# Optimization experiments

Hardware: AMD Instinct MI355X
Metric: run time of the kernel (lower is better)

Reference implementation:

```python
import jax, jax.numpy as jnp
import numpy as np

B, NPG, H, D = 16, 4096, 2, 64            # graphs, nodes/graph, heads, in_channels
N = B * NPG                                # 65536 total nodes
E_PER = 32768                              # edges per graph (avg degree 8)
E = B * E_PER                              # 524288 total edges
K_ORDER = 4
BETA = 0.5
D_OUT = 64


def setup_inputs():
    key = jax.random.key(0)
    k = jax.random.split(key, 10)
    x = jax.random.normal(k[0], (N, D), jnp.float32)
    # intra-graph random edges (block-diagonal adjacency)
    src = jax.random.randint(k[1], (B, E_PER), 0, NPG)
    dst = jax.random.randint(k[2], (B, E_PER), 0, NPG)
    off = (jnp.arange(B) * NPG)[:, None]
    edge_index = jnp.stack([(src + off).reshape(-1), (dst + off).reshape(-1)], axis=0)
    batch = jnp.arange(N) // NPG
    s = 1.0 / np.sqrt(D)
    Wq = jax.random.normal(k[3], (D, D * H), jnp.float32) * s
    bq = jnp.zeros((D * H,), jnp.float32)
    Wk = jax.random.normal(k[4], (D, D * H), jnp.float32) * s
    bk = jnp.zeros((D * H,), jnp.float32)
    Wo = jax.random.normal(k[5], (D * H, D_OUT), jnp.float32) * (1.0 / np.sqrt(D * H))
    bo = jnp.zeros((D_OUT,), jnp.float32)
    return {"x": x, "edge_index": edge_index, "batch": batch,
            "Wq": Wq, "bq": bq, "Wk": Wk, "bk": bk, "Wo": Wo, "bo": bo}


def reference(x, edge_index, batch, Wq, bq, Wk, bk, Wo, bo):
    Nn = x.shape[0]
    q = (x @ Wq + bq).reshape(Nn, H, D)
    k = (x @ Wk + bk).reshape(Nn, H, D)
    qs = q / jnp.linalg.norm(q, axis=2, keepdims=True)
    ks = k / jnp.linalg.norm(k, axis=2, keepdims=True)

    # symmetric-normalized transposed adjacency: adj_t[col_e, row_e] = w_e
    row, col = edge_index[0], edge_index[1]
    w = jnp.ones((row.shape[0],), x.dtype)
    deg = jax.ops.segment_sum(w, col, num_segments=N)
    dinv = jnp.where(deg > 0, deg ** -0.5, 0.0)
    val = dinv[col] * w * dinv[row]

    def gcn(xs):  # xs [N,H,D]; out[i] = sum_{e: col_e==i} val_e * xs[row_e]
        return jax.ops.segment_sum(val[:, None, None] * xs[row], col, num_segments=N)

    # ragged block <-> padded batch conversion (block-sorted batch ids)
    counts = jax.ops.segment_sum(jnp.ones((Nn,), jnp.int32), batch, num_segments=B)
    starts = jnp.concatenate([jnp.zeros((1,), jnp.int32), jnp.cumsum(counts)[:-1]])
    pos = jnp.arange(Nn) - starts[batch]

    def to_batch(v):
        return jnp.zeros((B, NPG) + v.shape[1:], v.dtype).at[batch, pos].set(v)

    def to_block(v):
        return v[batch, pos]

    qs_b, ks_b = to_batch(qs), to_batch(ks)      # [B, NPG, H, D]
    xs = jnp.broadcast_to(x[:, None, :], (Nn, H, D))
    xs_b = to_batch(xs)

    # linear (kernelized) attention; note source adds B (=qs.shape[0]) to the
    # denominator and uses the pre-loop xs_batch for every iteration -- kept faithful.
    kvs = jnp.einsum('blhm,blhd->bhmd', ks_b, xs_b)
    qkvs = jnp.einsum('bnhm,bhmd->bnhd', qs_b, kvs)
    num = qkvs + xs_b.sum(axis=1)[:, None]                       # [B,NPG,H,D]
    den = jnp.einsum('bnhm,bhm->bnh', qs_b, ks_b.sum(axis=1))[..., None] + float(B)
    attn_blk = to_block(num / den)                               # [N,H,D]

    for _ in range(K_ORDER):
        xs = xs + BETA * gcn(xs) + (1.0 - BETA) * attn_blk

    return (xs.reshape(Nn, H * D) @ Wo + bo) / H
```

## Files before the change

kernel.cpp:

```cpp
#include <hip/hip_runtime.h>

#define N_NODES 65536
#define B_G     16
#define NPG_    4096
#define H_H     2
#define D_D     64
#define HD      128
#define E_E     524288
#define D_OUT   64


__global__ void deg_kernel(const int* __restrict__ col, int* __restrict__ degi) {
    int e = blockIdx.x * 256 + threadIdx.x;
    if (e < E_E) atomicAdd(&degi[col[e]], 1);
}

__global__ void scan1(const int* __restrict__ degi, int* __restrict__ ptr,
                      int* __restrict__ bsums, float* __restrict__ dinv) {
    __shared__ int lds[256];
    int t = threadIdx.x;
    int i = blockIdx.x * 256 + t;
    int v = degi[i];
    dinv[i] = (v > 0) ? (1.0f / sqrtf((float)v)) : 0.0f;
    lds[t] = v;
    __syncthreads();
    for (int off = 1; off < 256; off <<= 1) {
        int tmp = (t >= off) ? lds[t - off] : 0;
        __syncthreads();
        lds[t] += tmp;
        __syncthreads();
    }
    ptr[i] = lds[t] - v;
    if (t == 255) bsums[blockIdx.x] = lds[255];
}

__global__ void scan3(int* __restrict__ ptr, const int* __restrict__ bsums) {
    __shared__ int red[256];
    int t = threadIdx.x;
    red[t] = (t < (int)blockIdx.x) ? bsums[t] : 0;
    __syncthreads();
    for (int off = 128; off > 0; off >>= 1) {
        if (t < off) red[t] += red[t + off];
        __syncthreads();
    }
    int i = blockIdx.x * 256 + t;
    ptr[i] += red[0];
    if (i == 0) ptr[N_NODES] = E_E;
}

__global__ void scatter_kernel(const int* __restrict__ row, const int* __restrict__ col,
                               const int* __restrict__ ptr, int* __restrict__ cursor,
                               const float* __restrict__ dinv,
                               int2* __restrict__ ep) {
    int e = blockIdx.x * 256 + threadIdx.x;
    if (e < E_E) {
        int c = col[e], r = row[e];
        int p = ptr[c] + atomicAdd(&cursor[c], 1);
        ep[p] = make_int2(r, __float_as_int(dinv[c] * dinv[r]));
    }
}

__global__ __launch_bounds__(256, 2) void proj_kernel(
    const float* __restrict__ x,
    const float* __restrict__ Wq, const float* __restrict__ bq,
    const float* __restrict__ Wk, const float* __restrict__ bk,
    float* __restrict__ qs, float* __restrict__ ks) {
    __shared__ float4 wt4[16 * 128];
    __shared__ float4 xt4[128 * 16];
    int t = threadIdx.x;
    int qk = blockIdx.x & 1;
    int nb = (blockIdx.x >> 1) * 128;
    const float* W = qk ? Wk : Wq;
    const float* bias = qk ? bk : bq;
    float* outp = qk ? ks : qs;

    for (int i = t; i < 2048; i += 256) {
        int k4 = i >> 7, c = i & 127;
        wt4[i] = make_float4(W[(4 * k4 + 0) * 128 + c], W[(4 * k4 + 1) * 128 + c],
                             W[(4 * k4 + 2) * 128 + c], W[(4 * k4 + 3) * 128 + c]);
    }
    const float4* xg = (const float4*)(x + (size_t)nb * 64);
    for (int i = t; i < 2048; i += 256) {
        int node = i >> 4, k4 = i & 15;
        xt4[node * 16 + (k4 ^ (node & 7))] = xg[i];
    }
    __syncthreads();

    int cg = t & 15;
    int ns = t >> 4;
    int sw = ns & 7;

    float acc[8][8];
#pragma unroll
    for (int i = 0; i < 8; ++i)
#pragma unroll
        for (int j = 0; j < 8; ++j) acc[i][j] = 0.f;

    for (int k4 = 0; k4 < 16; ++k4) {
        float4 wv[8];
#pragma unroll
        for (int j = 0; j < 8; ++j) wv[j] = wt4[k4 * 128 + cg + 16 * j];
        int kx = k4 ^ sw;
#pragma unroll
        for (int i = 0; i < 8; ++i) {
            float4 xv = xt4[(ns + 16 * i) * 16 + kx];
#pragma unroll
            for (int j = 0; j < 8; ++j)
                acc[i][j] += wv[j].x * xv.x + wv[j].y * xv.y +
                             wv[j].z * xv.z + wv[j].w * xv.w;
        }
    }

    float bcol[8];
#pragma unroll
    for (int j = 0; j < 8; ++j) bcol[j] = bias[cg + 16 * j];

#pragma unroll
    for (int i = 0; i < 8; ++i) {
#pragma unroll
        for (int j = 0; j < 8; ++j) acc[i][j] += bcol[j];
        float s0 = acc[i][0] * acc[i][0] + acc[i][1] * acc[i][1] +
                   acc[i][2] * acc[i][2] + acc[i][3] * acc[i][3];
        float s1 = acc[i][4] * acc[i][4] + acc[i][5] * acc[i][5] +
                   acc[i][6] * acc[i][6] + acc[i][7] * acc[i][7];
#pragma unroll
        for (int off = 8; off > 0; off >>= 1) {
            s0 += __shfl_xor(s0, off);
            s1 += __shfl_xor(s1, off);
        }
        float r0 = rsqrtf(s0), r1 = rsqrtf(s1);
        size_t base = (size_t)(nb + ns + 16 * i) * 128 + cg;
#pragma unroll
        for (int j = 0; j < 4; ++j) outp[base + 16 * j] = acc[i][j] * r0;
#pragma unroll
        for (int j = 4; j < 8; ++j) outp[base + 16 * j] = acc[i][j] * r1;
    }
}

__global__ __launch_bounds__(256) void kvs_part(
    const float* __restrict__ ks, const float* __restrict__ x,
    float* __restrict__ partials, float* __restrict__ ksum, float* __restrict__ xsum) {
    int bid = blockIdx.x;
    int chunk = bid & 31;
    int bh = bid >> 5;
    int b = bh >> 1, h = bh & 1;
    int t = threadIdx.x;
    int mrow = t >> 4, dcol = t & 15;
    int m0 = mrow * 4, d0 = dcol * 4;
    __shared__ float kl[32 * 64];
    __shared__ float xl[32 * 64];
    float acc[4][4] = {{0}};
    float ksacc[4] = {0, 0, 0, 0};
    float xsacc[4] = {0, 0, 0, 0};
    int node0 = b * NPG_ + chunk * 128;
    for (int s = 0; s < 4; ++s) {
        int nb = node0 + s * 32;
        for (int i = t; i < 512; i += 256) {
            int l = i >> 4, q = i & 15;
            ((float4*)kl)[i] = *(const float4*)(ks + (size_t)(nb + l) * 128 + h * 64 + q * 4);
        }
        const float4* xg = (const float4*)(x + (size_t)nb * 64);
        for (int i = t; i < 512; i += 256) ((float4*)xl)[i] = xg[i];
        __syncthreads();
        for (int l = 0; l < 32; ++l) {
            float4 kv = *(float4*)(kl + l * 64 + m0);
            float4 xv = *(float4*)(xl + l * 64 + d0);
            float kk[4] = {kv.x, kv.y, kv.z, kv.w};
            float xx[4] = {xv.x, xv.y, xv.z, xv.w};
#pragma unroll
            for (int i = 0; i < 4; ++i)
#pragma unroll
                for (int j = 0; j < 4; ++j) acc[i][j] += kk[i] * xx[j];
            if (dcol == 0) {
#pragma unroll
                for (int i = 0; i < 4; ++i) ksacc[i] += kk[i];
            }
            if (mrow == 0) {
#pragma unroll
                for (int j = 0; j < 4; ++j) xsacc[j] += xx[j];
            }
        }
        __syncthreads();
    }
    float* pout = partials + (size_t)bid * 4096;
#pragma unroll
    for (int i = 0; i < 4; ++i)
        *(float4*)(pout + (m0 + i) * 64 + d0) =
            make_float4(acc[i][0], acc[i][1], acc[i][2], acc[i][3]);
    if (dcol == 0) {
#pragma unroll
        for (int i = 0; i < 4; ++i) atomicAdd(&ksum[bh * 64 + m0 + i], ksacc[i]);
    }
    if (mrow == 0 && h == 0) {
#pragma unroll
        for (int j = 0; j < 4; ++j) atomicAdd(&xsum[b * 64 + d0 + j], xsacc[j]);
    }
}

__global__ __launch_bounds__(256) void kvs_reduce(
    const float* __restrict__ partials, float* __restrict__ kvs) {
    int i = blockIdx.x * 256 + threadIdx.x;
    int bh = i >> 12, elem = i & 4095;
    const float* p = partials + (size_t)bh * 32 * 4096 + elem;
    float s = 0.f;
#pragma unroll
    for (int c = 0; c < 32; ++c) s += p[c * 4096];
    kvs[i] = s;
}

__global__ __launch_bounds__(256, 3) void attn_kernel(
    const float* __restrict__ qs, const float* __restrict__ kvs,
    const float* __restrict__ ksum, const float* __restrict__ xsum,
    float* __restrict__ attn) {
    __shared__ float4 wt4[16 * 64];
    __shared__ float4 xt4[128 * 16];
    __shared__ float4 ksv[16];
    __shared__ float xsv[64];
    int bid = blockIdx.x;
    int h = bid & 1;
    int nb = (bid >> 1) * 128;
    int b = nb >> 12;
    int bh = b * 2 + h;
    int t = threadIdx.x;

    const float* kvp = kvs + (size_t)bh * 4096;
    for (int i = t; i < 1024; i += 256) {
        int k4 = i >> 6, d = i & 63;
        wt4[i] = make_float4(kvp[(4 * k4 + 0) * 64 + d], kvp[(4 * k4 + 1) * 64 + d],
                             kvp[(4 * k4 + 2) * 64 + d], kvp[(4 * k4 + 3) * 64 + d]);
    }
    for (int i = t; i < 2048; i += 256) {
        int node = i >> 4, k4 = i & 15;
        xt4[node * 16 + (k4 ^ (node & 7))] =
            *(const float4*)(qs + (size_t)(nb + node) * 128 + h * 64 + 4 * k4);
    }
    if (t < 16) ksv[t] = *(const float4*)(ksum + bh * 64 + 4 * t);
    if (t < 64) xsv[t] = xsum[b * 64 + t];
    __syncthreads();

    int cg = t & 15;
    int ns = t >> 4;
    int sw = ns & 7;

    float acc[8][4];
    float den[8];
#pragma unroll
    for (int i = 0; i < 8; ++i) {
        den[i] = 0.f;
#pragma unroll
        for (int j = 0; j < 4; ++j) acc[i][j] = 0.f;
    }

    for (int k4 = 0; k4 < 16; ++k4) {
        float4 kv = ksv[k4];
        float4 wv[4];
#pragma unroll
        for (int j = 0; j < 4; ++j) wv[j] = wt4[k4 * 64 + cg + 16 * j];
        int kx = k4 ^ sw;
#pragma unroll
        for (int i = 0; i < 8; ++i) {
            float4 xv = xt4[(ns + 16 * i) * 16 + kx];
            den[i] += kv.x * xv.x + kv.y * xv.y + kv.z * xv.z + kv.w * xv.w;
#pragma unroll
            for (int j = 0; j < 4; ++j)
                acc[i][j] += wv[j].x * xv.x + wv[j].y * xv.y +
                             wv[j].z * xv.z + wv[j].w * xv.w;
        }
    }

    float xs_d[4];
#pragma unroll
    for (int j = 0; j < 4; ++j) xs_d[j] = xsv[cg + 16 * j];

#pragma unroll
    for (int i = 0; i < 8; ++i) {
        float inv = 1.0f / (den[i] + 16.0f);
        size_t base = (size_t)(nb + ns + 16 * i) * 128 + h * 64 + cg;
#pragma unroll
        for (int j = 0; j < 4; ++j)
            attn[base + 16 * j] = (acc[i][j] + xs_d[j]) * inv;
    }
}

__global__ __launch_bounds__(256) void awo_kernel(
    const float* __restrict__ attn, const float* __restrict__ Wo,
    float* __restrict__ a) {
    __shared__ float4 wt4[32 * 64];
    __shared__ float4 xt4[64 * 32];
    int t = threadIdx.x;
    int nb = blockIdx.x * 64;

    for (int i = t; i < 2048; i += 256) {
        int k4 = i >> 6, c = i & 63;
        wt4[i] = make_float4(Wo[(4 * k4 + 0) * 64 + c], Wo[(4 * k4 + 1) * 64 + c],
                             Wo[(4 * k4 + 2) * 64 + c], Wo[(4 * k4 + 3) * 64 + c]);
    }
    const float4* ag = (const float4*)(attn + (size_t)nb * 128);
    for (int i = t; i < 2048; i += 256) xt4[i] = ag[i];
    __syncthreads();

    int cg = t & 15;
    int ns = t >> 4;
    int s = ns & 3;
    int n_t = ns * 4;

    float acc[4][4] = {{0.f}};
#pragma unroll 4
    for (int k4 = 0; k4 < 32; ++k4) {
        int kk = k4 ^ s;
        float4 xv0 = xt4[(n_t + 0) * 32 + kk];
        float4 xv1 = xt4[(n_t + 1) * 32 + kk];
        float4 xv2 = xt4[(n_t + 2) * 32 + kk];
        float4 xv3 = xt4[(n_t + 3) * 32 + kk];
#pragma unroll
        for (int j = 0; j < 4; ++j) {
            float4 wv = wt4[kk * 64 + cg + 16 * j];
            acc[0][j] += wv.x * xv0.x + wv.y * xv0.y + wv.z * xv0.z + wv.w * xv0.w;
            acc[1][j] += wv.x * xv1.x + wv.y * xv1.y + wv.z * xv1.z + wv.w * xv1.w;
            acc[2][j] += wv.x * xv2.x + wv.y * xv2.y + wv.z * xv2.z + wv.w * xv2.w;
            acc[3][j] += wv.x * xv3.x + wv.y * xv3.y + wv.z * xv3.z + wv.w * xv3.w;
        }
    }
#pragma unroll
    for (int i = 0; i < 4; ++i)
#pragma unroll
        for (int j = 0; j < 4; ++j)
            a[(size_t)(nb + n_t + i) * 64 + cg + 16 * j] = acc[i][j];
}

__global__ __launch_bounds__(256) void y0_kernel(
    const float* __restrict__ x, const float* __restrict__ Wo,
    float* __restrict__ y0) {
    __shared__ float4 wt4[16 * 64];
    __shared__ float4 xt4[64 * 16];
    int t = threadIdx.x;
    int nb = blockIdx.x * 64;

    for (int i = t; i < 1024; i += 256) {
        int k4 = i >> 6, c = i & 63;
        wt4[i] = make_float4(
            Wo[(4 * k4 + 0) * 64 + c] + Wo[(4 * k4 + 64) * 64 + c],
            Wo[(4 * k4 + 1) * 64 + c] + Wo[(4 * k4 + 65) * 64 + c],
            Wo[(4 * k4 + 2) * 64 + c] + Wo[(4 * k4 + 66) * 64 + c],
            Wo[(4 * k4 + 3) * 64 + c] + Wo[(4 * k4 + 67) * 64 + c]);
    }
    const float4* xg = (const float4*)(x + (size_t)nb * 64);
    for (int i = t; i < 1024; i += 256) xt4[i] = xg[i];
    __syncthreads();

    int cg = t & 15;
    int ns = t >> 4;
    int s = ns & 3;
    int n_t = ns * 4;

    float acc[4][4] = {{0.f}};
#pragma unroll 4
    for (int k4 = 0; k4 < 16; ++k4) {
        int kk = k4 ^ s;
        float4 xv0 = xt4[(n_t + 0) * 16 + kk];
        float4 xv1 = xt4[(n_t + 1) * 16 + kk];
        float4 xv2 = xt4[(n_t + 2) * 16 + kk];
        float4 xv3 = xt4[(n_t + 3) * 16 + kk];
#pragma unroll
        for (int j = 0; j < 4; ++j) {
            float4 wv = wt4[kk * 64 + cg + 16 * j];
            acc[0][j] += wv.x * xv0.x + wv.y * xv0.y + wv.z * xv0.z + wv.w * xv0.w;
            acc[1][j] += wv.x * xv1.x + wv.y * xv1.y + wv.z * xv1.z + wv.w * xv1.w;
            acc[2][j] += wv.x * xv2.x + wv.y * xv2.y + wv.z * xv2.z + wv.w * xv2.w;
            acc[3][j] += wv.x * xv3.x + wv.y * xv3.y + wv.z * xv3.z + wv.w * xv3.w;
        }
    }
#pragma unroll
    for (int i = 0; i < 4; ++i)
#pragma unroll
        for (int j = 0; j < 4; ++j)
            y0[(size_t)(nb + n_t + i) * 64 + cg + 16 * j] = acc[i][j];
}

template <int LAST>
__global__ __launch_bounds__(256) void gcn64_kernel(
    const float* __restrict__ yin, const float* __restrict__ a,
    const int* __restrict__ ptr, const int2* __restrict__ ep,
    float* __restrict__ yout, const float* __restrict__ bo) {
    int bid = blockIdx.x;
    int lbid = (bid & 7) * (N_NODES / 16 / 8) + (bid >> 3);
    int t = threadIdx.x;
    int n = lbid * 16 + (t >> 4);
    int lg = t & 15;
    int c4 = lg * 4;
    int e0 = ptr[n], e1 = ptr[n + 1];
    int cnt = e1 - e0;
    float4 acc = make_float4(0.f, 0.f, 0.f, 0.f);

    int2 q[16];
#pragma unroll
    for (int i = 0; i < 16; ++i) {
        int ee = e0 + i;
        if (ee > e1 - 1) ee = e1 - 1;
        if (ee < 0) ee = 0;
        q[i] = ep[ee];
    }
#pragma unroll
    for (int i = 0; i < 16; ++i) {
        if (i < cnt) {
            float v = __int_as_float(q[i].y);
            float4 xv = *(const float4*)(yin + (size_t)q[i].x * 64 + c4);
            acc.x += v * xv.x; acc.y += v * xv.y;
            acc.z += v * xv.z; acc.w += v * xv.w;
        }
    }
    for (int e = e0 + 16; e < e1; ++e) {
        int2 qq = ep[e];
        float v = __int_as_float(qq.y);
        float4 xv = *(const float4*)(yin + (size_t)qq.x * 64 + c4);
        acc.x += v * xv.x; acc.y += v * xv.y;
        acc.z += v * xv.z; acc.w += v * xv.w;
    }

    size_t idx = (size_t)n * 64 + c4;
    float4 self = *(const float4*)(yin + idx);
    float4 at = *(const float4*)(a + idx);
    float4 o;
    o.x = self.x + 0.5f * acc.x + 0.5f * at.x;
    o.y = self.y + 0.5f * acc.y + 0.5f * at.y;
    o.z = self.z + 0.5f * acc.z + 0.5f * at.z;
    o.w = self.w + 0.5f * acc.w + 0.5f * at.w;
    if (LAST) {
        float4 bv = *(const float4*)(bo + c4);
        o.x = (o.x + bv.x) * 0.5f;
        o.y = (o.y + bv.y) * 0.5f;
        o.z = (o.z + bv.z) * 0.5f;
        o.w = (o.w + bv.w) * 0.5f;
    }
    *(float4*)(yout + idx) = o;
}


extern "C" void kernel_launch(void* const* d_in, const int* in_sizes, int n_in,
                              void* d_out, int out_size, void* d_ws, size_t ws_size,
                              hipStream_t stream) {
    const float* x  = (const float*)d_in[0];
    const int* ei   = (const int*)d_in[1];
    const float* Wq = (const float*)d_in[3];
    const float* bq = (const float*)d_in[4];
    const float* Wk = (const float*)d_in[5];
    const float* bk = (const float*)d_in[6];
    const float* Wo = (const float*)d_in[7];
    const float* bo = (const float*)d_in[8];
    float* out = (float*)d_out;

    const int* row = ei;
    const int* col = ei + E_E;

    float* bufA = (float*)d_ws;
    float* bufB = bufA + (size_t)N_NODES * HD;
    float* bufC = bufB + (size_t)N_NODES * HD;
    int2*  ep   = (int2*)(bufC + (size_t)N_NODES * HD);
    float* kvs  = (float*)(ep + E_E);
    float* ksum = kvs + 131072;
    float* xsum = ksum + 2048;
    float* dinv = xsum + 1024;
    int* degi   = (int*)(dinv + N_NODES);
    int* cursor = degi + N_NODES;
    int* ptr    = cursor + N_NODES;
    int* bsums  = ptr + N_NODES + 1;

    float* a_  = bufA;
    float* yA  = bufA + (size_t)N_NODES * 64;
    float* yB  = bufB;

    hipMemsetAsync(degi, 0, (size_t)N_NODES * 2 * 4, stream);
    hipMemsetAsync(ksum, 0, (size_t)(2048 + 1024) * 4, stream);

    deg_kernel<<<E_E / 256, 256, 0, stream>>>(col, degi);
    scan1<<<N_NODES / 256, 256, 0, stream>>>(degi, ptr, bsums, dinv);
    scan3<<<N_NODES / 256, 256, 0, stream>>>(ptr, bsums);
    scatter_kernel<<<E_E / 256, 256, 0, stream>>>(row, col, ptr, cursor, dinv, ep);

    proj_kernel<<<1024, 256, 0, stream>>>(x, Wq, bq, Wk, bk, bufA, bufB);

    kvs_part<<<1024, 256, 0, stream>>>(bufB, x, bufC, ksum, xsum);
    kvs_reduce<<<512, 256, 0, stream>>>(bufC, kvs);
    attn_kernel<<<1024, 256, 0, stream>>>(bufA, kvs, ksum, xsum, bufC);

    awo_kernel<<<1024, 256, 0, stream>>>(bufC, Wo, a_);
    y0_kernel<<<1024, 256, 0, stream>>>(x, Wo, yA);

    gcn64_kernel<0><<<N_NODES / 16, 256, 0, stream>>>(yA, a_, ptr, ep, yB, bo);
    gcn64_kernel<0><<<N_NODES / 16, 256, 0, stream>>>(yB, a_, ptr, ep, yA, bo);
    gcn64_kernel<0><<<N_NODES / 16, 256, 0, stream>>>(yA, a_, ptr, ep, yB, bo);
    gcn64_kernel<1><<<N_NODES / 16, 256, 0, stream>>>(yB, a_, ptr, ep, out, bo);
}
```

Baseline: 359.7 us.

## Fold Wo into kv state and fuse attention with output projection

A new small kernel precomputes M = kvs·Wo_h and C = xsum·Wo_h per graph and head. The attention kernel then projects qs directly through M, so it writes only the 64-wide projected attention and never materialises the 128-wide attention buffer that awo_kernel used to read back. The projection kernel is also split per head into 2048 blocks, with half the accumulators and no dual-launch-bounds hint. This removes one full pass over an N×128 intermediate, at the cost of an extra tiny kernel launch and some buffer reassignment.

```diff
diff --git a/kernel.cpp b/kernel.cpp
--- a/kernel.cpp
+++ b/kernel.cpp
@@ -60,24 +60,26 @@
     }
 }
 
-__global__ __launch_bounds__(256, 2) void proj_kernel(
+__global__ __launch_bounds__(256) void proj_kernel(
     const float* __restrict__ x,
     const float* __restrict__ Wq, const float* __restrict__ bq,
     const float* __restrict__ Wk, const float* __restrict__ bk,
     float* __restrict__ qs, float* __restrict__ ks) {
-    __shared__ float4 wt4[16 * 128];
+    __shared__ float4 wt4[16 * 64];
     __shared__ float4 xt4[128 * 16];
     int t = threadIdx.x;
     int qk = blockIdx.x & 1;
-    int nb = (blockIdx.x >> 1) * 128;
+    int hh = (blockIdx.x >> 1) & 1;
+    int nb = (blockIdx.x >> 2) * 128;
     const float* W = qk ? Wk : Wq;
     const float* bias = qk ? bk : bq;
     float* outp = qk ? ks : qs;
 
-    for (int i = t; i < 2048; i += 256) {
-        int k4 = i >> 7, c = i & 127;
-        wt4[i] = make_float4(W[(4 * k4 + 0) * 128 + c], W[(4 * k4 + 1) * 128 + c],
-                             W[(4 * k4 + 2) * 128 + c], W[(4 * k4 + 3) * 128 + c]);
+    for (int i = t; i < 1024; i += 256) {
+        int k4 = i >> 6, c = i & 63;
+        int cc = hh * 64 + c;
+        wt4[i] = make_float4(W[(4 * k4 + 0) * 128 + cc], W[(4 * k4 + 1) * 128 + cc],
+                             W[(4 * k4 + 2) * 128 + cc], W[(4 * k4 + 3) * 128 + cc]);
     }
     const float4* xg = (const float4*)(x + (size_t)nb * 64);
     for (int i = t; i < 2048; i += 256) {
@@ -90,50 +92,43 @@
     int ns = t >> 4;
     int sw = ns & 7;
 
-    float acc[8][8];
+    float acc[8][4];
 #pragma unroll
     for (int i = 0; i < 8; ++i)
 #pragma unroll
-        for (int j = 0; j < 8; ++j) acc[i][j] = 0.f;
+        for (int j = 0; j < 4; ++j) acc[i][j] = 0.f;
 
     for (int k4 = 0; k4 < 16; ++k4) {
-        float4 wv[8];
-#pragma unroll
-        for (int j = 0; j < 8; ++j) wv[j] = wt4[k4 * 128 + cg + 16 * j];
+        float4 wv[4];
+#pragma unroll
+        for (int j = 0; j < 4; ++j) wv[j] = wt4[k4 * 64 + cg + 16 * j];
         int kx = k4 ^ sw;
 #pragma unroll
         for (int i = 0; i < 8; ++i) {
             float4 xv = xt4[(ns + 16 * i) * 16 + kx];
 #pragma unroll
-            for (int j = 0; j < 8; ++j)
+            for (int j = 0; j < 4; ++j)
                 acc[i][j] += wv[j].x * xv.x + wv[j].y * xv.y +
                              wv[j].z * xv.z + wv[j].w * xv.w;
         }
     }
 
-    float bcol[8];
-#pragma unroll
-    for (int j = 0; j < 8; ++j) bcol[j] = bias[cg + 16 * j];
+    float bcol[4];
+#pragma unroll
+    for (int j = 0; j < 4; ++j) bcol[j] = bias[hh * 64 + cg + 16 * j];
 
 #pragma unroll
     for (int i = 0; i < 8; ++i) {
 #pragma unroll
-        for (int j = 0; j < 8; ++j) acc[i][j] += bcol[j];
-        float s0 = acc[i][0] * acc[i][0] + acc[i][1] * acc[i][1] +
-                   acc[i][2] * acc[i][2] + acc[i][3] * acc[i][3];
-        float s1 = acc[i][4] * acc[i][4] + acc[i][5] * acc[i][5] +
-                   acc[i][6] * acc[i][6] + acc[i][7] * acc[i][7];
-#pragma unroll
-        for (int off = 8; off > 0; off >>= 1) {
-            s0 += __shfl_xor(s0, off);
-            s1 += __shfl_xor(s1, off);
-        }
-        float r0 = rsqrtf(s0), r1 = rsqrtf(s1);
-        size_t base = (size_t)(nb + ns + 16 * i) * 128 + cg;
-#pragma unroll
-        for (int j = 0; j < 4; ++j) outp[base + 16 * j] = acc[i][j] * r0;
-#pragma unroll
-        for (int j = 4; j < 8; ++j) outp[base + 16 * j] = acc[i][j] * r1;
+        for (int j = 0; j < 4; ++j) acc[i][j] += bcol[j];
+        float s = acc[i][0] * acc[i][0] + acc[i][1] * acc[i][1] +
+                  acc[i][2] * acc[i][2] + acc[i][3] * acc[i][3];
+#pragma unroll
+        for (int off = 8; off > 0; off >>= 1) s += __shfl_xor(s, off);
+        float r = rsqrtf(s);
+        size_t base = (size_t)(nb + ns + 16 * i) * 128 + hh * 64 + cg;
+#pragma unroll
+        for (int j = 0; j < 4; ++j) outp[base + 16 * j] = acc[i][j] * r;
     }
 }
 
@@ -208,119 +203,117 @@
     kvs[i] = s;
 }
 
-__global__ __launch_bounds__(256, 3) void attn_kernel(
-    const float* __restrict__ qs, const float* __restrict__ kvs,
-    const float* __restrict__ ksum, const float* __restrict__ xsum,
-    float* __restrict__ attn) {
+__global__ __launch_bounds__(256) void mwo_kernel(
+    const float* __restrict__ kvs, const float* __restrict__ Wo,
+    const float* __restrict__ xsum, float* __restrict__ M, float* __restrict__ C) {
+    __shared__ float kv_l[64 * 64];
+    __shared__ float wo_l[64 * 64];
+    __shared__ float xs_l[64];
+    int bh = blockIdx.x;
+    int b = bh >> 1, h = bh & 1;
+    int t = threadIdx.x;
+    const float4* kvg = (const float4*)(kvs + (size_t)bh * 4096);
+    for (int i = t; i < 1024; i += 256) ((float4*)kv_l)[i] = kvg[i];
+    for (int i = t; i < 1024; i += 256) {
+        int d = i >> 4;
+        ((float4*)wo_l)[i] = *(const float4*)(Wo + (size_t)(h * 64 + d) * 64 + (i & 15) * 4);
+    }
+    if (t < 64) xs_l[t] = xsum[b * 64 + t];
+    __syncthreads();
+
+    int ccol = t & 15, mrow = t >> 4;
+    int m0 = mrow * 4, c0 = ccol * 4;
+    float acc[4][4] = {{0.f}};
+    float cacc[4] = {0.f, 0.f, 0.f, 0.f};
+    for (int d = 0; d < 64; ++d) {
+        float4 wv = *(const float4*)(wo_l + d * 64 + c0);
+        float kvv[4];
+#pragma unroll
+        for (int i = 0; i < 4; ++i) kvv[i] = kv_l[(m0 + i) * 64 + d];
+#pragma unroll
+        for (int i = 0; i < 4; ++i) {
+            acc[i][0] += kvv[i] * wv.x; acc[i][1] += kvv[i] * wv.y;
+            acc[i][2] += kvv[i] * wv.z; acc[i][3] += kvv[i] * wv.w;
+        }
+        if (mrow == 0) {
+            float xv = xs_l[d];
+            cacc[0] += xv * wv.x; cacc[1] += xv * wv.y;
+            cacc[2] += xv * wv.z; cacc[3] += xv * wv.w;
+        }
+    }
+    float* mo = M + (size_t)bh * 4096;
+#pragma unroll
+    for (int i = 0; i < 4; ++i)
+        *(float4*)(mo + (m0 + i) * 64 + c0) =
+            make_float4(acc[i][0], acc[i][1], acc[i][2], acc[i][3]);
+    if (mrow == 0)
+        *(float4*)(C + bh * 64 + c0) = make_float4(cacc[0], cacc[1], cacc[2], cacc[3]);
+}
+
+__global__ __launch_bounds__(256) void fatt_kernel(
+    const float* __restrict__ qs, const float* __restrict__ M,
+    const float* __restrict__ C, const float* __restrict__ ksum,
+    float* __restrict__ a) {
     __shared__ float4 wt4[16 * 64];
-    __shared__ float4 xt4[128 * 16];
+    __shared__ float4 xt4[64 * 16];
     __shared__ float4 ksv[16];
-    __shared__ float xsv[64];
-    int bid = blockIdx.x;
-    int h = bid & 1;
-    int nb = (bid >> 1) * 128;
+    __shared__ float csv[64];
+    int nb = blockIdx.x * 64;
     int b = nb >> 12;
-    int bh = b * 2 + h;
-    int t = threadIdx.x;
-
-    const float* kvp = kvs + (size_t)bh * 4096;
-    for (int i = t; i < 1024; i += 256) {
-        int k4 = i >> 6, d = i & 63;
-        wt4[i] = make_float4(kvp[(4 * k4 + 0) * 64 + d], kvp[(4 * k4 + 1) * 64 + d],
-                             kvp[(4 * k4 + 2) * 64 + d], kvp[(4 * k4 + 3) * 64 + d]);
-    }
-    for (int i = t; i < 2048; i += 256) {
-        int node = i >> 4, k4 = i & 15;
-        xt4[node * 16 + (k4 ^ (node & 7))] =
-            *(const float4*)(qs + (size_t)(nb + node) * 128 + h * 64 + 4 * k4);
-    }
-    if (t < 16) ksv[t] = *(const float4*)(ksum + bh * 64 + 4 * t);
-    if (t < 64) xsv[t] = xsum[b * 64 + t];
-    __syncthreads();
-
+    int t = threadIdx.x;
     int cg = t & 15;
     int ns = t >> 4;
-    int sw = ns & 7;
-
-    float acc[8][4];
-    float den[8];
-#pragma unroll
-    for (int i = 0; i < 8; ++i) {
-        den[i] = 0.f;
-#pragma unroll
-        for (int j = 0; j < 4; ++j) acc[i][j] = 0.f;
-    }
-
-    for (int k4 = 0; k4 < 16; ++k4) {
-        float4 kv = ksv[k4];
-        float4 wv[4];
-#pragma unroll
-        for (int j = 0; j < 4; ++j) wv[j] = wt4[k4 * 64 + cg + 16 * j];
-        int kx = k4 ^ sw;
-#pragma unroll
-        for (int i = 0; i < 8; ++i) {
-            float4 xv = xt4[(ns + 16 * i) * 16 + kx];
-            den[i] += kv.x * xv.x + kv.y * xv.y + kv.z * xv.z + kv.w * xv.w;
-#pragma unroll
-            for (int j = 0; j < 4; ++j)
-                acc[i][j] += wv[j].x * xv.x + wv[j].y * xv.y +
-                             wv[j].z * xv.z + wv[j].w * xv.w;
-        }
-    }
-
-    float xs_d[4];
-#pragma unroll
-    for (int j = 0; j < 4; ++j) xs_d[j] = xsv[cg + 16 * j];
-
-#pragma unroll
-    for (int i = 0; i < 8; ++i) {
-        float inv = 1.0f / (den[i] + 16.0f);
-        size_t base = (size_t)(nb + ns + 16 * i) * 128 + h * 64 + cg;
-#pragma unroll
-        for (int j = 0; j < 4; ++j)
-            attn[base + 16 * j] = (acc[i][j] + xs_d[j]) * inv;
-    }
-}
-
-__global__ __launch_bounds__(256) void awo_kernel(
-    const float* __restrict__ attn, const float* __restrict__ Wo,
-    float* __restrict__ a) {
-    __shared__ float4 wt4[32 * 64];
-    __shared__ float4 xt4[64 * 32];
-    int t = threadIdx.x;
-    int nb = blockIdx.x * 64;
-
-    for (int i = t; i < 2048; i += 256) {
-        int k4 = i >> 6, c = i & 63;
-        wt4[i] = make_float4(Wo[(4 * k4 + 0) * 64 + c], Wo[(4 * k4 + 1) * 64 + c],
-                             Wo[(4 * k4 + 2) * 64 + c], Wo[(4 * k4 + 3) * 64 + c]);
-    }
-    const float4* ag = (const float4*)(attn + (size_t)nb * 128);
-    for (int i = t; i < 2048; i += 256) xt4[i] = ag[i];
-    __syncthreads();
-
-    int cg = t & 15;
-    int ns = t >> 4;
-    int s = ns & 3;
+    int sw = ns & 3;
     int n_t = ns * 4;
 
     float acc[4][4] = {{0.f}};
-#pragma unroll 4
-    for (int k4 = 0; k4 < 32; ++k4) {
-        int kk = k4 ^ s;
-        float4 xv0 = xt4[(n_t + 0) * 32 + kk];
-        float4 xv1 = xt4[(n_t + 1) * 32 + kk];
-        float4 xv2 = xt4[(n_t + 2) * 32 + kk];
-        float4 xv3 = xt4[(n_t + 3) * 32 + kk];
-#pragma unroll
-        for (int j = 0; j < 4; ++j) {
-            float4 wv = wt4[kk * 64 + cg + 16 * j];
-            acc[0][j] += wv.x * xv0.x + wv.y * xv0.y + wv.z * xv0.z + wv.w * xv0.w;
-            acc[1][j] += wv.x * xv1.x + wv.y * xv1.y + wv.z * xv1.z + wv.w * xv1.w;
-            acc[2][j] += wv.x * xv2.x + wv.y * xv2.y + wv.z * xv2.z + wv.w * xv2.w;
-            acc[3][j] += wv.x * xv3.x + wv.y * xv3.y + wv.z * xv3.z + wv.w * xv3.w;
-        }
-    }
+
+    for (int h = 0; h < 2; ++h) {
+        int bh = b * 2 + h;
+        const float* mp = M + (size_t)bh * 4096;
+        for (int i = t; i < 1024; i += 256) {
+            int k4 = i >> 6, c = i & 63;
+            wt4[i] = make_float4(mp[(4 * k4 + 0) * 64 + c], mp[(4 * k4 + 1) * 64 + c],
+                                 mp[(4 * k4 + 2) * 64 + c], mp[(4 * k4 + 3) * 64 + c]);
+        }
+        for (int i = t; i < 1024; i += 256) {
+            int node = i >> 4, k4 = i & 15;
+            xt4[i] = *(const float4*)(qs + (size_t)(nb + node) * 128 + h * 64 + 4 * k4);
+        }
+        if (t < 16) ksv[t] = *(const float4*)(ksum + bh * 64 + 4 * t);
+        if (t < 64) csv[t] = C[bh * 64 + t];
+        __syncthreads();
+
+        float pacc[4][4] = {{0.f}};
+        float den[4] = {0.f, 0.f, 0.f, 0.f};
+        for (int k4 = 0; k4 < 16; ++k4) {
+            int kk = k4 ^ sw;
+            float4 kv = ksv[kk];
+            float4 wv[4];
+#pragma unroll
+            for (int j = 0; j < 4; ++j) wv[j] = wt4[kk * 64 + cg + 16 * j];
+#pragma unroll
+            for (int i = 0; i < 4; ++i) {
+                float4 xv = xt4[(n_t + i) * 16 + kk];
+                den[i] += kv.x * xv.x + kv.y * xv.y + kv.z * xv.z + kv.w * xv.w;
+#pragma unroll
+                for (int j = 0; j < 4; ++j)
+                    pacc[i][j] += wv[j].x * xv.x + wv[j].y * xv.y +
+                                  wv[j].z * xv.z + wv[j].w * xv.w;
+            }
+        }
+        float cc[4];
+#pragma unroll
+        for (int j = 0; j < 4; ++j) cc[j] = csv[cg + 16 * j];
+#pragma unroll
+        for (int i = 0; i < 4; ++i) {
+            float inv = 1.0f / (den[i] + 16.0f);
+#pragma unroll
+            for (int j = 0; j < 4; ++j) acc[i][j] += (pacc[i][j] + cc[j]) * inv;
+        }
+        __syncthreads();
+    }
+
 #pragma unroll
     for (int i = 0; i < 4; ++i)
 #pragma unroll
@@ -457,7 +450,9 @@
     float* bufC = bufB + (size_t)N_NODES * HD;
     int2*  ep   = (int2*)(bufC + (size_t)N_NODES * HD);
     float* kvs  = (float*)(ep + E_E);
-    float* ksum = kvs + 131072;
+    float* M    = kvs + 131072;
+    float* Cc   = M + 131072;
+    float* ksum = Cc + 2048;
     float* xsum = ksum + 2048;
     float* dinv = xsum + 1024;
     int* degi   = (int*)(dinv + N_NODES);
@@ -465,9 +460,12 @@
     int* ptr    = cursor + N_NODES;
     int* bsums  = ptr + N_NODES + 1;
 
-    float* a_  = bufA;
-    float* yA  = bufA + (size_t)N_NODES * 64;
-    float* yB  = bufB;
+    float* qs_      = bufC;
+    float* ks_      = bufB;
+    float* a_       = bufA;
+    float* yA       = bufA + (size_t)N_NODES * 64;
+    float* partials = yA;
+    float* yB       = bufB;
 
     hipMemsetAsync(degi, 0, (size_t)N_NODES * 2 * 4, stream);
     hipMemsetAsync(ksum, 0, (size_t)(2048 + 1024) * 4, stream);
@@ -477,13 +475,13 @@
     scan3<<<N_NODES / 256, 256, 0, stream>>>(ptr, bsums);
     scatter_kernel<<<E_E / 256, 256, 0, stream>>>(row, col, ptr, cursor, dinv, ep);
 
-    proj_kernel<<<1024, 256, 0, stream>>>(x, Wq, bq, Wk, bk, bufA, bufB);
-
-    kvs_part<<<1024, 256, 0, stream>>>(bufB, x, bufC, ksum, xsum);
-    kvs_reduce<<<512, 256, 0, stream>>>(bufC, kvs);
-    attn_kernel<<<1024, 256, 0, stream>>>(bufA, kvs, ksum, xsum, bufC);
-
-    awo_kernel<<<1024, 256, 0, stream>>>(bufC, Wo, a_);
+    proj_kernel<<<2048, 256, 0, stream>>>(x, Wq, bq, Wk, bk, qs_, ks_);
+
+    kvs_part<<<1024, 256, 0, stream>>>(ks_, x, partials, ksum, xsum);
+    kvs_reduce<<<512, 256, 0, stream>>>(partials, kvs);
+    mwo_kernel<<<32, 256, 0, stream>>>(kvs, Wo, xsum, M, Cc);
+    fatt_kernel<<<1024, 256, 0, stream>>>(qs_, M, Cc, ksum, a_);
+
     y0_kernel<<<1024, 256, 0, stream>>>(x, Wo, yA);
 
     gcn64_kernel<0><<<N_NODES / 16, 256, 0, stream>>>(yA, a_, ptr, ep, yB, bo);
```

Result: faster. 336.3 us (-6.5%).
